# Optimization experiments

Measured on AMD Instinct MI355X. Metric: run time of the kernel, lower is better.

The kernel has to match this reference:

```python
import jax, jax.numpy as jnp
import numpy as np

B, T, D, N_ITER, SR = 32, 1024, 1024, 256, 4


def setup_inputs() -> dict:
    key = jax.random.key(0)
    k1, k2 = jax.random.split(key)
    xs = jax.random.normal(k1, (B, T, D), dtype=jnp.float32)
    ds = jax.random.uniform(k2, (B, T, N_ITER), dtype=jnp.float32)
    return {"xs": xs, "ds": ds, "is_inference": 1}


def _linear_interp(d, f):
    # d: (B, T) velocity field sampled on the integer grid; f: (B, T) fractional positions
    Tn = d.shape[-1]
    i0 = jnp.clip(jnp.floor(f).astype(jnp.int32), 0, Tn - 2)
    t = f - i0.astype(f.dtype)
    d0 = jnp.take_along_axis(d, i0, axis=-1)
    d1 = jnp.take_along_axis(d, i0 + 1, axis=-1)
    return d0 + t * (d1 - d0)


def _gw_ode(ds):
    # ds: (B, T, N) per-step warp increments (already divided by N*sr).
    # m=1 init: f = identity grid + first field; then N-1 Euler steps f += d_i(f).
    Bb, Tn, N = ds.shape
    grid = jnp.arange(Tn, dtype=ds.dtype)[None, :]
    f0 = jnp.clip(grid + ds[:, :, 0], 0.0, Tn - 1.0)

    def step(f, d):
        f = jnp.clip(f + _linear_interp(d, f), 0.0, Tn - 1.0)
        return f, None

    d_steps = jnp.moveaxis(ds[:, :, 1:], -1, 0)  # (N-1, B, T)
    f, _ = jax.lax.scan(step, f0, d_steps)
    return f


def _cubic_interpolation(x, f):
    # Catmull-Rom cubic resampling. x: (B, D, T) channel-first; f: (B, T) positions.
    Tn = x.shape[-1]
    i1 = jnp.clip(jnp.floor(f).astype(jnp.int32), 0, Tn - 1)
    t = (f - i1.astype(f.dtype))[:, None, :]  # (B, 1, T)

    def gat(idx):
        idx = jnp.clip(idx, 0, Tn - 1)
        return jnp.take_along_axis(x, jnp.broadcast_to(idx[:, None, :], x.shape), axis=-1)

    p0, p1, p2, p3 = gat(i1 - 1), gat(i1), gat(i1 + 1), gat(i1 + 2)
    t2 = t * t
    t3 = t2 * t
    w0 = -0.5 * t3 + t2 - 0.5 * t
    w1 = 1.5 * t3 - 2.5 * t2 + 1.0
    w2 = -1.5 * t3 + 2.0 * t2 + 0.5 * t
    w3 = 0.5 * t3 - 0.5 * t2
    return w0 * p0 + w1 * p1 + w2 * p2 + w3 * p3


def reference(xs, ds, is_inference):
    ds = ds / (ds.shape[-1] * SR)
    f = _gw_ode(ds)                                   # (B, T) warp function
    ys = _cubic_interpolation(jnp.swapaxes(xs, -1, -2), f)  # (B, D, T)
    return jnp.swapaxes(ys, -1, -2), f
```

## Files before the change

kernel.cpp:

```cpp
#include <hip/hip_runtime.h>

#define BB 32
#define TT 1024
#define DD 1024
#define NIT 256
#define SRR 4
#define CS 32
#define K1T 128

typedef float vf4 __attribute__((ext_vector_type(4)));

__global__ __launch_bounds__(K1T) void gw_ode_kernel(const float* __restrict__ ds,
                                                     float* __restrict__ f_out) {
    __shared__ float slab[(K1T + 1) * 33];
    const int tid = threadIdx.x;
    const int b   = blockIdx.x >> 3;
    const int t0  = (blockIdx.x & 7) * K1T;
    const int t   = t0 + tid;
    const int r0  = (t < TT - 2) ? t : (TT - 2);
    const int ia  = r0 - t0;
    const float inv = 1.0f / (float)(NIT * SRR);
    const float lo  = -(float)r0;
    const float hi  = (float)(TT - 1 - r0);
    const bool edge = (r0 == TT - 2);

    const float4* dsv = (const float4*)ds;

    float4 buf[2][9];
#pragma unroll
    for (int it = 0; it < 8; ++it) {
        const int p = it * K1T + tid, r = p >> 3, q = p & 7;
        const int row = (t0 + r < TT - 1) ? (t0 + r) : (TT - 1);
        buf[0][it] = dsv[(size_t)(b * TT + row) * (NIT / 4) + q];
    }
    if (tid < 8) {
        const int row = (t0 + K1T < TT - 1) ? (t0 + K1T) : (TT - 1);
        buf[0][8] = dsv[(size_t)(b * TT + row) * (NIT / 4) + tid];
    }

    float g = 0.0f;
    bool bad = false;

#pragma unroll
    for (int c = 0; c < NIT / CS; ++c) {
        if (c > 0) __syncthreads();
#pragma unroll
        for (int it = 0; it < 8; ++it) {
            const int p = it * K1T + tid, r = p >> 3, q = p & 7;
            const float4 v = buf[c & 1][it];
            float* s = slab + r * 33 + q * 4;
            s[0] = v.x; s[1] = v.y; s[2] = v.z; s[3] = v.w;
        }
        if (tid < 8) {
            const float4 v = buf[c & 1][8];
            float* s = slab + K1T * 33 + tid * 4;
            s[0] = v.x; s[1] = v.y; s[2] = v.z; s[3] = v.w;
        }
        __syncthreads();
        if (c < NIT / CS - 1) {
#pragma unroll
            for (int it = 0; it < 8; ++it) {
                const int p = it * K1T + tid, r = p >> 3, q = p & 7;
                const int row = (t0 + r < TT - 1) ? (t0 + r) : (TT - 1);
                buf[(c + 1) & 1][it] =
                    dsv[(size_t)(b * TT + row) * (NIT / 4) + (c + 1) * (CS / 4) + q];
            }
            if (tid < 8) {
                const int row = (t0 + K1T < TT - 1) ? (t0 + K1T) : (TT - 1);
                buf[(c + 1) & 1][8] =
                    dsv[(size_t)(b * TT + row) * (NIT / 4) + (c + 1) * (CS / 4) + tid];
            }
        }
        int jstart = 0;
        if (c == 0) {
            float f0 = (float)t + slab[tid * 33] * inv;
            f0 = fminf(fmaxf(f0, 0.0f), (float)(TT - 1));
            g = f0 - (float)r0;
            jstart = 1;
        }
#pragma unroll 8
        for (int j = jstart; j < CS; ++j) {
            const float d0 = slab[ia * 33 + j] * inv;
            const float d1 = slab[(ia + 1) * 33 + j] * inv;
            g = fmaf(g, 1.0f + (d1 - d0), d0);
            g = fminf(fmaxf(g, lo), hi);
            bad |= (g < 0.0f) | ((g >= 1.0f) & !(edge & (g == hi)));
        }
    }

    float fres = (float)r0 + g;
    if (bad) {
        float f = (float)t + ds[(size_t)(b * TT + t) * NIT] * inv;
        f = fminf(fmaxf(f, 0.0f), (float)(TT - 1));
        for (int i = 1; i < NIT; ++i) {
            int i0 = (int)floorf(f);
            i0 = min(max(i0, 0), TT - 2);
            const float d0 = ds[(size_t)(b * TT + i0) * NIT + i] * inv;
            const float d1 = ds[(size_t)(b * TT + i0 + 1) * NIT + i] * inv;
            const float tf = f - (float)i0;
            f = fminf(fmaxf(f + d0 + tf * (d1 - d0), 0.0f), (float)(TT - 1));
        }
        fres = f;
    }
    f_out[b * TT + t] = fres;
}

__global__ __launch_bounds__(256) void cubic_kernel(const float* __restrict__ xs,
                                                    const float* __restrict__ f_in,
                                                    float* __restrict__ out) {
    const int nwg = BB * TT;
    const int bt = (blockIdx.x & 7) * (nwg >> 3) + (blockIdx.x >> 3);
    const int b = bt >> 10;

    const float fv = f_in[bt];
    int i1 = (int)floorf(fv);
    i1 = min(max(i1, 0), TT - 1);
    const float tf = fv - (float)i1;
    const float t2 = tf * tf;
    const float t3 = t2 * tf;
    const float w0 = -0.5f * t3 + t2 - 0.5f * tf;
    const float w1 = 1.5f * t3 - 2.5f * t2 + 1.0f;
    const float w2 = -1.5f * t3 + 2.0f * t2 + 0.5f * tf;
    const float w3 = 0.5f * t3 - 0.5f * t2;

    const int j0 = max(i1 - 1, 0);
    const int j2 = min(i1 + 1, TT - 1);
    const int j3 = min(i1 + 2, TT - 1);

    const size_t base = (size_t)b * TT * DD;
    const float4* r0 = (const float4*)(xs + base + (size_t)j0 * DD);
    const float4* r1 = (const float4*)(xs + base + (size_t)i1 * DD);
    const float4* r2 = (const float4*)(xs + base + (size_t)j2 * DD);
    const float4* r3 = (const float4*)(xs + base + (size_t)j3 * DD);
    vf4* o = (vf4*)(out + (size_t)bt * DD);

    const int d = threadIdx.x;
    const float4 p0 = r0[d];
    const float4 p1 = r1[d];
    const float4 p2 = r2[d];
    const float4 p3 = r3[d];
    vf4 v;
    v.x = w0 * p0.x + w1 * p1.x + w2 * p2.x + w3 * p3.x;
    v.y = w0 * p0.y + w1 * p1.y + w2 * p2.y + w3 * p3.y;
    v.z = w0 * p0.z + w1 * p1.z + w2 * p2.z + w3 * p3.z;
    v.w = w0 * p0.w + w1 * p1.w + w2 * p2.w + w3 * p3.w;
    __builtin_nontemporal_store(v, &o[d]);
}

extern "C" void kernel_launch(void* const* d_in, const int* in_sizes, int n_in,
                              void* d_out, int out_size, void* d_ws, size_t ws_size,
                              hipStream_t stream) {
    const float* xs = (const float*)d_in[0];
    const float* ds = (const float*)d_in[1];

    float* out_ys = (float*)d_out;
    float* out_f  = out_ys + (size_t)BB * TT * DD;

    gw_ode_kernel<<<dim3((BB * TT) / K1T), K1T, 0, stream>>>(ds, out_f);
    cubic_kernel<<<dim3(BB * TT), 256, 0, stream>>>(xs, out_f, out_ys);
}
```

Baseline: 54.76 us.

## Fuse warp ODE and cubic resampling into a single kernel per time tile

```diff
diff --git a/kernel.cpp b/kernel.cpp
--- a/kernel.cpp
+++ b/kernel.cpp
@@ -5,146 +5,111 @@
 #define DD 1024
 #define NIT 256
 #define SRR 4
-#define CS 32
-#define K1T 128
+#define KT 16
+#define SLDA 261
 
 typedef float vf4 __attribute__((ext_vector_type(4)));
 
-__global__ __launch_bounds__(K1T) void gw_ode_kernel(const float* __restrict__ ds,
-                                                     float* __restrict__ f_out) {
-    __shared__ float slab[(K1T + 1) * 33];
+__global__ __launch_bounds__(256, 4) void fused_kernel(const float* __restrict__ xs,
+                                                       const float* __restrict__ ds,
+                                                       float* __restrict__ out_ys,
+                                                       float* __restrict__ f_out) {
+    __shared__ float slab[(KT + 1) * SLDA];
+    __shared__ float fbuf[KT];
+
+    const int nwg = BB * (TT / KT);
+    const int blk = (blockIdx.x & 7) * (nwg >> 3) + (blockIdx.x >> 3);
+    const int b  = blk >> 6;
+    const int t0 = (blk & 63) * KT;
     const int tid = threadIdx.x;
-    const int b   = blockIdx.x >> 3;
-    const int t0  = (blockIdx.x & 7) * K1T;
-    const int t   = t0 + tid;
-    const int r0  = (t < TT - 2) ? t : (TT - 2);
-    const int ia  = r0 - t0;
     const float inv = 1.0f / (float)(NIT * SRR);
-    const float lo  = -(float)r0;
-    const float hi  = (float)(TT - 1 - r0);
-    const bool edge = (r0 == TT - 2);
 
     const float4* dsv = (const float4*)ds;
-
-    float4 buf[2][9];
 #pragma unroll
-    for (int it = 0; it < 8; ++it) {
-        const int p = it * K1T + tid, r = p >> 3, q = p & 7;
-        const int row = (t0 + r < TT - 1) ? (t0 + r) : (TT - 1);
-        buf[0][it] = dsv[(size_t)(b * TT + row) * (NIT / 4) + q];
-    }
-    if (tid < 8) {
-        const int row = (t0 + K1T < TT - 1) ? (t0 + K1T) : (TT - 1);
-        buf[0][8] = dsv[(size_t)(b * TT + row) * (NIT / 4) + tid];
-    }
-
-    float g = 0.0f;
-    bool bad = false;
-
-#pragma unroll
-    for (int c = 0; c < NIT / CS; ++c) {
-        if (c > 0) __syncthreads();
-#pragma unroll
-        for (int it = 0; it < 8; ++it) {
-            const int p = it * K1T + tid, r = p >> 3, q = p & 7;
-            const float4 v = buf[c & 1][it];
-            float* s = slab + r * 33 + q * 4;
+    for (int it = 0; it < 5; ++it) {
+        const int idx = it * 256 + tid;
+        if (idx < (KT + 1) * (NIT / 4)) {
+            const int r = idx >> 6, q = idx & 63;
+            const int row = min(t0 + r, TT - 1);
+            const float4 v = dsv[((size_t)(b * TT + row) << 6) + q];
+            float* s = slab + r * SLDA + q * 4;
             s[0] = v.x; s[1] = v.y; s[2] = v.z; s[3] = v.w;
         }
-        if (tid < 8) {
-            const float4 v = buf[c & 1][8];
-            float* s = slab + K1T * 33 + tid * 4;
-            s[0] = v.x; s[1] = v.y; s[2] = v.z; s[3] = v.w;
-        }
-        __syncthreads();
-        if (c < NIT / CS - 1) {
-#pragma unroll
-            for (int it = 0; it < 8; ++it) {
-                const int p = it * K1T + tid, r = p >> 3, q = p & 7;
-                const int row = (t0 + r < TT - 1) ? (t0 + r) : (TT - 1);
-                buf[(c + 1) & 1][it] =
-                    dsv[(size_t)(b * TT + row) * (NIT / 4) + (c + 1) * (CS / 4) + q];
-            }
-            if (tid < 8) {
-                const int row = (t0 + K1T < TT - 1) ? (t0 + K1T) : (TT - 1);
-                buf[(c + 1) & 1][8] =
-                    dsv[(size_t)(b * TT + row) * (NIT / 4) + (c + 1) * (CS / 4) + tid];
-            }
-        }
-        int jstart = 0;
-        if (c == 0) {
-            float f0 = (float)t + slab[tid * 33] * inv;
-            f0 = fminf(fmaxf(f0, 0.0f), (float)(TT - 1));
-            g = f0 - (float)r0;
-            jstart = 1;
-        }
+    }
+    __syncthreads();
+
+    if (tid < KT) {
+        const int t  = t0 + tid;
+        const int r0 = (t < TT - 2) ? t : (TT - 2);
+        const int ia = r0 - t0;
+        const float lo = -(float)r0;
+        const float hi = (float)(TT - 1 - r0);
+        const bool edge = (r0 == TT - 2);
+
+        float f0 = (float)t + slab[tid * SLDA] * inv;
+        f0 = fminf(fmaxf(f0, 0.0f), (float)(TT - 1));
+        float g = f0 - (float)r0;
+        bool bad = false;
+
+        const float* s0 = slab + ia * SLDA;
+        const float* s1 = s0 + SLDA;
 #pragma unroll 8
-        for (int j = jstart; j < CS; ++j) {
-            const float d0 = slab[ia * 33 + j] * inv;
-            const float d1 = slab[(ia + 1) * 33 + j] * inv;
+        for (int i = 1; i < NIT; ++i) {
+            const float d0 = s0[i] * inv;
+            const float d1 = s1[i] * inv;
             g = fmaf(g, 1.0f + (d1 - d0), d0);
             g = fminf(fmaxf(g, lo), hi);
             bad |= (g < 0.0f) | ((g >= 1.0f) & !(edge & (g == hi)));
         }
+
+        float fres = (float)r0 + g;
+        if (bad) {
+            float f = (float)t + ds[(size_t)(b * TT + t) * NIT] * inv;
+            f = fminf(fmaxf(f, 0.0f), (float)(TT - 1));
+            for (int i = 1; i < NIT; ++i) {
+                int i0 = (int)floorf(f);
+                i0 = min(max(i0, 0), TT - 2);
+                const float d0 = ds[(size_t)(b * TT + i0) * NIT + i] * inv;
+                const float d1 = ds[(size_t)(b * TT + i0 + 1) * NIT + i] * inv;
+                const float tf = f - (float)i0;
+                f = fminf(fmaxf(f + d0 + tf * (d1 - d0), 0.0f), (float)(TT - 1));
+            }
+            fres = f;
+        }
+        fbuf[tid] = fres;
+        f_out[b * TT + t] = fres;
     }
+    __syncthreads();
 
-    float fres = (float)r0 + g;
-    if (bad) {
-        float f = (float)t + ds[(size_t)(b * TT + t) * NIT] * inv;
-        f = fminf(fmaxf(f, 0.0f), (float)(TT - 1));
-        for (int i = 1; i < NIT; ++i) {
-            int i0 = (int)floorf(f);
-            i0 = min(max(i0, 0), TT - 2);
-            const float d0 = ds[(size_t)(b * TT + i0) * NIT + i] * inv;
-            const float d1 = ds[(size_t)(b * TT + i0 + 1) * NIT + i] * inv;
-            const float tf = f - (float)i0;
-            f = fminf(fmaxf(f + d0 + tf * (d1 - d0), 0.0f), (float)(TT - 1));
-        }
-        fres = f;
+    const float4* X = (const float4*)xs + (size_t)b * TT * (DD / 4);
+    vf4* O = (vf4*)out_ys;
+
+    for (int k = 0; k < KT; ++k) {
+        const float fv = fbuf[k];
+        int i1 = (int)floorf(fv);
+        i1 = min(max(i1, 0), TT - 1);
+        const float tf = fv - (float)i1;
+        const float t2 = tf * tf, t3 = t2 * tf;
+        const float w0 = -0.5f * t3 + t2 - 0.5f * tf;
+        const float w1 = 1.5f * t3 - 2.5f * t2 + 1.0f;
+        const float w2 = -1.5f * t3 + 2.0f * t2 + 0.5f * tf;
+        const float w3 = 0.5f * t3 - 0.5f * t2;
+
+        const int j0 = max(i1 - 1, 0);
+        const int j2 = min(i1 + 1, TT - 1);
+        const int j3 = min(i1 + 2, TT - 1);
+
+        const float4 p0 = X[((size_t)j0 << 8) + tid];
+        const float4 p1 = X[((size_t)i1 << 8) + tid];
+        const float4 p2 = X[((size_t)j2 << 8) + tid];
+        const float4 p3 = X[((size_t)j3 << 8) + tid];
+        vf4 v;
+        v.x = w0 * p0.x + w1 * p1.x + w2 * p2.x + w3 * p3.x;
+        v.y = w0 * p0.y + w1 * p1.y + w2 * p2.y + w3 * p3.y;
+        v.z = w0 * p0.z + w1 * p1.z + w2 * p2.z + w3 * p3.z;
+        v.w = w0 * p0.w + w1 * p1.w + w2 * p2.w + w3 * p3.w;
+        __builtin_nontemporal_store(v, O + (((size_t)(b * TT + t0 + k)) << 8) + tid);
     }
-    f_out[b * TT + t] = fres;
-}
-
-__global__ __launch_bounds__(256) void cubic_kernel(const float* __restrict__ xs,
-                                                    const float* __restrict__ f_in,
-                                                    float* __restrict__ out) {
-    const int nwg = BB * TT;
-    const int bt = (blockIdx.x & 7) * (nwg >> 3) + (blockIdx.x >> 3);
-    const int b = bt >> 10;
-
-    const float fv = f_in[bt];
-    int i1 = (int)floorf(fv);
-    i1 = min(max(i1, 0), TT - 1);
-    const float tf = fv - (float)i1;
-    const float t2 = tf * tf;
-    const float t3 = t2 * tf;
-    const float w0 = -0.5f * t3 + t2 - 0.5f * tf;
-    const float w1 = 1.5f * t3 - 2.5f * t2 + 1.0f;
-    const float w2 = -1.5f * t3 + 2.0f * t2 + 0.5f * tf;
-    const float w3 = 0.5f * t3 - 0.5f * t2;
-
-    const int j0 = max(i1 - 1, 0);
-    const int j2 = min(i1 + 1, TT - 1);
-    const int j3 = min(i1 + 2, TT - 1);
-
-    const size_t base = (size_t)b * TT * DD;
-    const float4* r0 = (const float4*)(xs + base + (size_t)j0 * DD);
-    const float4* r1 = (const float4*)(xs + base + (size_t)i1 * DD);
-    const float4* r2 = (const float4*)(xs + base + (size_t)j2 * DD);
-    const float4* r3 = (const float4*)(xs + base + (size_t)j3 * DD);
-    vf4* o = (vf4*)(out + (size_t)bt * DD);
-
-    const int d = threadIdx.x;
-    const float4 p0 = r0[d];
-    const float4 p1 = r1[d];
-    const float4 p2 = r2[d];
-    const float4 p3 = r3[d];
-    vf4 v;
-    v.x = w0 * p0.x + w1 * p1.x + w2 * p2.x + w3 * p3.x;
-    v.y = w0 * p0.y + w1 * p1.y + w2 * p2.y + w3 * p3.y;
-    v.z = w0 * p0.z + w1 * p1.z + w2 * p2.z + w3 * p3.z;
-    v.w = w0 * p0.w + w1 * p1.w + w2 * p2.w + w3 * p3.w;
-    __builtin_nontemporal_store(v, &o[d]);
 }
 
 extern "C" void kernel_launch(void* const* d_in, const int* in_sizes, int n_in,
@@ -156,6 +121,5 @@
     float* out_ys = (float*)d_out;
     float* out_f  = out_ys + (size_t)BB * TT * DD;
 
-    gw_ode_kernel<<<dim3((BB * TT) / K1T), K1T, 0, stream>>>(ds, out_f);
-    cubic_kernel<<<dim3(BB * TT), 256, 0, stream>>>(xs, out_f, out_ys);
+    fused_kernel<<<dim3(BB * (TT / KT)), 256, 0, stream>>>(xs, ds, out_ys, out_f);
 }
```

After: 62.71 us. 1.15x slower.
